# Kernel tuning notes

Measured on AMD Instinct MI355X. Metric: run time of the kernel, lower is better.

The kernel has to match this reference:

```python
import jax, jax.numpy as jnp
import numpy as np

D = 8192          # dimension (high_dim_mode since > 1000)
M = 1_600_000     # ~0.05 * D*(D-1) pairs after the i>j mask
RIEMANN_SHIFT = 0.5


def _lower_tri_pairs(rng, d, m):
    # Sample m unique strictly-lower-triangular (i, j) positions (i > j).
    total = d * (d - 1) // 2
    k = rng.choice(total, size=m, replace=False)
    kf = k.astype(np.float64)
    i = np.floor((1.0 + np.sqrt(1.0 + 8.0 * kf)) / 2.0).astype(np.int64)
    # fix possible off-by-one from float sqrt
    tri = i * (i - 1) // 2
    i = np.where(tri > k, i - 1, i)
    tri = i * (i - 1) // 2
    j = k - tri
    return i, j


def setup_inputs() -> dict:
    key = jax.random.key(0)
    k1, k2 = jax.random.split(key)
    rng = np.random.default_rng(0)

    i, j = _lower_tri_pairs(rng, D, M)
    interaction_indices = jnp.asarray(np.stack([i, j]))  # [2, M] int64

    local_scale = 1.0 / D ** 0.75
    h_local = jax.random.normal(k1, (D,), dtype=jnp.float32) * local_scale + RIEMANN_SHIFT

    dim_factor = 1.0 / (D ** 0.9 * np.log(D))
    V_interaction = jax.random.normal(k2, (M,), dtype=jnp.float32) * dim_factor

    return {
        "h_local": h_local,
        "V_interaction": V_interaction,
        "interaction_indices": interaction_indices,
        "dimension": D,
    }


def reference(h_local, V_interaction, interaction_indices, dimension) -> jnp.ndarray:
    d = h_local.shape[0]
    # scatter interaction values into strict lower triangle (set semantics,
    # indices are unique so set == torch assignment)
    H_int = jnp.zeros((d, d), dtype=h_local.dtype)
    H_int = H_int.at[interaction_indices[0], interaction_indices[1]].set(V_interaction)
    H_int = H_int + H_int.T  # symmetrize
    interaction_scale = 1.0 - 0.2 / np.sqrt(np.log(dimension))
    return jnp.diag(h_local) + H_int * interaction_scale
```

## Files before the change

kernel.cpp:

```cpp
#include <hip/hip_runtime.h>
#include <math.h>


#define P1_PAIRS 4096
#define NBKT     2048
#define BCAP     8
#define NB2      4096
#define OVB      512
#define OVCAP    64
#define SENTK    0xFFFFFFFFu
#define GCAP     65536


__global__ __launch_bounds__(1024) void p1_kernel(
    const int*   __restrict__ idx,
    const float* __restrict__ vals,
    float scale, int m, int nblk,
    uint2* __restrict__ region1,
    uint2* __restrict__ ovfreg,
    int*   __restrict__ ovfcur,
    uint2* __restrict__ glist,
    int*   __restrict__ ghdr)
{
    __shared__ uint2 stage[NBKT][BCAP];
    __shared__ int   cnt[NBKT];
    __shared__ uint2 ovfst[OVB];
    __shared__ int   ovfn;

    uint2* sflat = &stage[0][0];
    for (int f = threadIdx.x; f < NBKT * BCAP; f += 1024)
        sflat[f] = make_uint2(SENTK, 0u);
    for (int b = threadIdx.x; b < NBKT; b += 1024) cnt[b] = 0;
    if (threadIdx.x == 0) ovfn = 0;
    __syncthreads();

    const int blk  = blockIdx.x;
    const int base = blk * P1_PAIRS;
#pragma unroll
    for (int it = 0; it < P1_PAIRS / 1024; ++it) {
        int k = base + it * 1024 + threadIdx.x;
        if (k < m) {
            int i = idx[k];
            int j = idx[m + k];
            unsigned vb = __float_as_uint(vals[k] * scale);

            unsigned k1 = ((unsigned)i << 13) | (unsigned)j;
            int b1 = i >> 2;
            int p = atomicAdd(&cnt[b1], 1);
            if (p < BCAP) stage[b1][p] = make_uint2(k1, vb);
            else { int q = atomicAdd(&ovfn, 1);
                   if (q < OVB) ovfst[q] = make_uint2(k1, vb);
                   else { int g = atomicAdd(ghdr, 1); if (g < GCAP) glist[g] = make_uint2(k1, vb); } }

            unsigned k2 = ((unsigned)j << 13) | (unsigned)i;
            int b2 = j >> 2;
            p = atomicAdd(&cnt[b2], 1);
            if (p < BCAP) stage[b2][p] = make_uint2(k2, vb);
            else { int q = atomicAdd(&ovfn, 1);
                   if (q < OVB) ovfst[q] = make_uint2(k2, vb);
                   else { int g = atomicAdd(ghdr, 1); if (g < GCAP) glist[g] = make_uint2(k2, vb); } }
        }
    }
    __syncthreads();

    for (int f = threadIdx.x; f < NBKT * BCAP; f += 1024) {
        int b = f >> 3, e = f & 7;
        region1[((long long)b * nblk + blk) * BCAP + e] = sflat[f];
    }
    int n = ovfn; if (n > OVB) n = OVB;
    for (int e = threadIdx.x; e < n; e += 1024) {
        uint2 en = ovfst[e];
        int band2 = en.x >> 14;
        int pos = atomicAdd(&ovfcur[band2], 1);
        if (pos < OVCAP) ovfreg[band2 * OVCAP + pos] = en;
        else { int g = atomicAdd(ghdr, 1); if (g < GCAP) glist[g] = en; }
    }
}

__global__ __launch_bounds__(512) void p2_kernel(
    float* __restrict__ out,
    const float* __restrict__ h_local,
    const uint2* __restrict__ region1,
    int nblk,
    const uint2* __restrict__ ovfreg,
    const int*   __restrict__ ovfcur,
    const uint2* __restrict__ glist,
    const int*   __restrict__ ghdr)
{
    __shared__ float srow[2 * 8192];
    float4* s4 = reinterpret_cast<float4*>(srow);
    const int band2 = blockIdx.x;

    for (int c = threadIdx.x; c < 4096; c += 512)
        s4[c] = make_float4(0.f, 0.f, 0.f, 0.f);
    __syncthreads();

    const uint4* src = reinterpret_cast<const uint4*>(
        region1 + (long long)(band2 >> 1) * nblk * BCAP);
    const int n2 = (nblk * BCAP) >> 1;
    const unsigned bu = (unsigned)band2;
    for (int e = threadIdx.x; e < n2; e += 512) {
        uint4 en = src[e];
        if ((en.x >> 14) == bu) srow[en.x & 16383] = __uint_as_float(en.y);
        if ((en.z >> 14) == bu) srow[en.z & 16383] = __uint_as_float(en.w);
    }
    int n = ovfcur[band2]; if (n > OVCAP) n = OVCAP;
    for (int e = threadIdx.x; e < n; e += 512) {
        uint2 en = ovfreg[band2 * OVCAP + e];
        srow[en.x & 16383] = __uint_as_float(en.y);
    }
    int gn = ghdr[0];
    if (gn > 0) {
        if (gn > GCAP) gn = GCAP;
        for (int e = threadIdx.x; e < gn; e += 512) {
            uint2 en = glist[e];
            if ((en.x >> 14) == bu) srow[en.x & 16383] = __uint_as_float(en.y);
        }
    }
    if (threadIdx.x < 2) {
        int r = (band2 << 1) + threadIdx.x;
        srow[((unsigned)threadIdx.x << 13) | (unsigned)r] = h_local[r];
    }
    __syncthreads();

    float4* orow = reinterpret_cast<float4*>(out + ((long long)band2 << 14));
    for (int c = threadIdx.x; c < 4096; c += 512)
        orow[c] = s4[c];
}


__global__ __launch_bounds__(256) void init_counts_kernel(
    float* __restrict__ out, int d, int logd)
{
    int r = blockIdx.x * blockDim.x + threadIdx.x;
    if (r < d) reinterpret_cast<int*>(out)[(long long)r << logd] = 0;
}

__global__ __launch_bounds__(256) void bin_kernel(
    float* __restrict__ out,
    const int*   __restrict__ idx,
    const float* __restrict__ vals,
    float scale, int m, int logd, int cap)
{
    int k = blockIdx.x * blockDim.x + threadIdx.x;
    if (k >= m) return;
    int i = idx[k];
    int j = idx[m + k];
    unsigned vb = __float_as_uint(vals[k] * scale);
    int* cnt_i = reinterpret_cast<int*>(out) + ((long long)i << logd);
    int* cnt_j = reinterpret_cast<int*>(out) + ((long long)j << logd);
    int p1 = atomicAdd(cnt_i, 1);
    if (p1 < cap)
        *reinterpret_cast<uint2*>(out + ((long long)i << logd) + 2 + 2 * p1) =
            make_uint2((unsigned)j, vb);
    int p2 = atomicAdd(cnt_j, 1);
    if (p2 < cap)
        *reinterpret_cast<uint2*>(out + ((long long)j << logd) + 2 + 2 * p2) =
            make_uint2((unsigned)i, vb);
}

__global__ __launch_bounds__(256) void rows_kernel(
    float* __restrict__ out,
    const float* __restrict__ h_local,
    int logd, int cap)
{
    __shared__ float srow[8192];
    const int d  = 1 << logd;
    const int n4 = d >> 2;
    float4* s4 = reinterpret_cast<float4*>(srow);
    const int r = blockIdx.x;
    float* grow = out + ((long long)r << logd);
    const float4 z = make_float4(0.f, 0.f, 0.f, 0.f);
    for (int c = threadIdx.x; c < n4; c += blockDim.x) s4[c] = z;
    __syncthreads();
    int cnt = reinterpret_cast<const int*>(grow)[0];
    if (cnt > cap) cnt = cap;
    const uint2* eb = reinterpret_cast<const uint2*>(grow + 2);
    for (int e = threadIdx.x; e < cnt; e += blockDim.x) {
        uint2 p = eb[e];
        srow[p.x] = __uint_as_float(p.y);
    }
    if (threadIdx.x == 0) srow[r] = h_local[r];
    __syncthreads();
    for (int c = threadIdx.x; c < n4; c += blockDim.x)
        reinterpret_cast<float4*>(grow)[c] = s4[c];
}

__global__ __launch_bounds__(256) void fill_diag_kernel(
    float* __restrict__ out, const float* __restrict__ h_local,
    int d, long long n)
{
    long long t = (long long)blockIdx.x * blockDim.x + threadIdx.x;
    if (t >= n) return;
    long long row = t / d;
    long long col = t - row * d;
    out[t] = (row == col) ? h_local[row] : 0.f;
}

__global__ __launch_bounds__(256) void scatter_kernel(
    float* __restrict__ out,
    const int* __restrict__ idx,
    const float* __restrict__ vals,
    float scale, int m, int d)
{
    int k = blockIdx.x * blockDim.x + threadIdx.x;
    if (k >= m) return;
    int i = idx[k];
    int j = idx[m + k];
    float v = vals[k] * scale;
    out[(long long)i * d + j] = v;
    out[(long long)j * d + i] = v;
}


extern "C" void kernel_launch(void* const* d_in, const int* in_sizes, int n_in,
                              void* d_out, int out_size, void* d_ws, size_t ws_size,
                              hipStream_t stream) {
    const float* h_local = (const float*)d_in[0];
    const float* V_int   = (const float*)d_in[1];
    const int*   idx     = (const int*)d_in[2];

    const int d = in_sizes[0];
    const int m = in_sizes[1];

    int logd = 0;
    while ((1 << logd) < d) ++logd;
    const bool pow2 = ((1 << logd) == d);

    const float iscale = (float)(1.0 - 0.2 / sqrt(log((double)d)));
    float* out = (float*)d_out;
    const int block = 256;

    const int nblk = (m + P1_PAIRS - 1) / P1_PAIRS;

    const size_t off_ovfcur = 4096;
    const size_t hdr_bytes  = off_ovfcur + (size_t)NB2 * 4;
    const size_t off_glist  = 24576;
    const size_t off_ovfreg = off_glist + (size_t)GCAP * sizeof(uint2);
    const size_t off_r1     = off_ovfreg + (size_t)NB2 * OVCAP * sizeof(uint2);
    const size_t ws_need    = off_r1 + (size_t)NBKT * nblk * BCAP * sizeof(uint2);

    const bool path7 = (d == 8192) && (m > 0) && (m <= 2000000) &&
                       (d_ws != nullptr) && (ws_size >= ws_need);

    if (path7) {
        char* ws = (char*)d_ws;
        int*   ghdr    = (int*)ws;
        int*   ovfcur  = (int*)(ws + off_ovfcur);
        uint2* glist   = (uint2*)(ws + off_glist);
        uint2* ovfreg  = (uint2*)(ws + off_ovfreg);
        uint2* region1 = (uint2*)(ws + off_r1);

        hipMemsetAsync(ws, 0, hdr_bytes, stream);
        p1_kernel<<<nblk, 1024, 0, stream>>>(idx, V_int, iscale, m, nblk,
                                             region1, ovfreg, ovfcur, glist, ghdr);
        p2_kernel<<<NB2, 512, 0, stream>>>(out, h_local, region1, nblk,
                                           ovfreg, ovfcur, glist, ghdr);
    } else if (pow2 && d >= 1024 && d <= 8192 &&
               ((long long)m * 2 / d) < (long long)((d - 2) / 2) / 2) {
        const int cap = (d - 2) / 2;
        init_counts_kernel<<<(d + block - 1) / block, block, 0, stream>>>(out, d, logd);
        bin_kernel<<<(m + block - 1) / block, block, 0, stream>>>(out, idx, V_int,
                                                                  iscale, m, logd, cap);
        rows_kernel<<<d, block, 0, stream>>>(out, h_local, logd, cap);
    } else {
        const long long n = (long long)d * d;
        const long long grid_fill = (n + block - 1) / block;
        fill_diag_kernel<<<(dim3)(unsigned)grid_fill, block, 0, stream>>>(out, h_local, d, n);
        const int grid_sc = (m + block - 1) / block;
        scatter_kernel<<<grid_sc, block, 0, stream>>>(out, idx, V_int, iscale, m, d);
    }
}
```

Before: 328.2 us.

## Use fixed chunk count in binning and double-buffer multi-band row assembly

The binning pass now uses a fixed 512 chunks of about 3125 pairs each, two chunks per 1024-thread block, in place of fixed 4096-pair blocks. The row-assembly kernel now handles 16 bands per 1024-thread block and ping-pongs two shared buffers. It writes one band to global memory and zeroes that buffer while gathering the next band into the other. This is meant to cut launch and per-block zero-init overhead and to overlap gather reads with output writes. The risks are 256 p2 blocks, which may leave CUs underused, and the 8-slot buckets, which now see more pairs per chunk and so may overflow more often.

Result: slower. 349.1 us (+6.4%).

```diff
diff --git a/kernel.cpp b/kernel.cpp
--- a/kernel.cpp
+++ b/kernel.cpp
@@ -2,10 +2,11 @@
 #include <math.h>
 
 
-#define P1_PAIRS 4096
+#define NCHUNK   512
 #define NBKT     2048
 #define BCAP     8
 #define NB2      4096
+#define BANDS_PB 16
 #define OVB      512
 #define OVCAP    64
 #define SENTK    0xFFFFFFFFu
@@ -15,7 +16,7 @@
 __global__ __launch_bounds__(1024) void p1_kernel(
     const int*   __restrict__ idx,
     const float* __restrict__ vals,
-    float scale, int m, int nblk,
+    float scale, int m, int cs,
     uint2* __restrict__ region1,
     uint2* __restrict__ ovfreg,
     int*   __restrict__ ovfcur,
@@ -26,20 +27,20 @@
     __shared__ int   cnt[NBKT];
     __shared__ uint2 ovfst[OVB];
     __shared__ int   ovfn;
-
     uint2* sflat = &stage[0][0];
-    for (int f = threadIdx.x; f < NBKT * BCAP; f += 1024)
-        sflat[f] = make_uint2(SENTK, 0u);
-    for (int b = threadIdx.x; b < NBKT; b += 1024) cnt[b] = 0;
-    if (threadIdx.x == 0) ovfn = 0;
-    __syncthreads();
-
-    const int blk  = blockIdx.x;
-    const int base = blk * P1_PAIRS;
-#pragma unroll
-    for (int it = 0; it < P1_PAIRS / 1024; ++it) {
-        int k = base + it * 1024 + threadIdx.x;
-        if (k < m) {
+    const int tid = threadIdx.x;
+
+    for (int c = 0; c < 2; ++c) {
+        const int chunk = blockIdx.x * 2 + c;
+
+        for (int f = tid; f < NBKT * BCAP; f += 1024) sflat[f] = make_uint2(SENTK, 0u);
+        for (int b = tid; b < NBKT; b += 1024) cnt[b] = 0;
+        if (tid == 0) ovfn = 0;
+        __syncthreads();
+
+        const int base = chunk * cs;
+        int end = base + cs; if (end > m) end = m;
+        for (int k = base + tid; k < end; k += 1024) {
             int i = idx[k];
             int j = idx[m + k];
             unsigned vb = __float_as_uint(vals[k] * scale);
@@ -60,72 +61,101 @@
                    if (q < OVB) ovfst[q] = make_uint2(k2, vb);
                    else { int g = atomicAdd(ghdr, 1); if (g < GCAP) glist[g] = make_uint2(k2, vb); } }
         }
-    }
-    __syncthreads();
-
-    for (int f = threadIdx.x; f < NBKT * BCAP; f += 1024) {
-        int b = f >> 3, e = f & 7;
-        region1[((long long)b * nblk + blk) * BCAP + e] = sflat[f];
-    }
-    int n = ovfn; if (n > OVB) n = OVB;
-    for (int e = threadIdx.x; e < n; e += 1024) {
-        uint2 en = ovfst[e];
-        int band2 = en.x >> 14;
-        int pos = atomicAdd(&ovfcur[band2], 1);
-        if (pos < OVCAP) ovfreg[band2 * OVCAP + pos] = en;
-        else { int g = atomicAdd(ghdr, 1); if (g < GCAP) glist[g] = en; }
-    }
-}
-
-__global__ __launch_bounds__(512) void p2_kernel(
+        __syncthreads();
+
+        for (int f = tid; f < NBKT * BCAP; f += 1024) {
+            int bkt = f >> 3, e = f & 7;
+            region1[((long long)bkt * NCHUNK + chunk) * BCAP + e] = sflat[f];
+        }
+        int n = ovfn; if (n > OVB) n = OVB;
+        for (int e = tid; e < n; e += 1024) {
+            uint2 en = ovfst[e];
+            int band = en.x >> 14;
+            int pos = atomicAdd(&ovfcur[band], 1);
+            if (pos < OVCAP) ovfreg[band * OVCAP + pos] = en;
+            else { int g = atomicAdd(ghdr, 1); if (g < GCAP) glist[g] = en; }
+        }
+        __syncthreads();
+    }
+}
+
+__device__ __forceinline__ void gather_band(
+    float* __restrict__ buf,
+    int band,
+    const uint2* __restrict__ region1,
+    const uint2* __restrict__ ovfreg,
+    const int*   __restrict__ ovfcur,
+    const uint2* __restrict__ glist,
+    int gn,
+    const float* __restrict__ h_local,
+    int tid)
+{
+    const uint4* src = reinterpret_cast<const uint4*>(
+        region1 + (long long)(band >> 1) * NCHUNK * BCAP);
+    const unsigned bu = (unsigned)band;
+    for (int e = tid; e < (NCHUNK * BCAP) / 2; e += 1024) {
+        uint4 en = src[e];
+        if ((en.x >> 14) == bu) buf[en.x & 16383] = __uint_as_float(en.y);
+        if ((en.z >> 14) == bu) buf[en.z & 16383] = __uint_as_float(en.w);
+    }
+    int n = ovfcur[band]; if (n > OVCAP) n = OVCAP;
+    for (int e = tid; e < n; e += 1024) {
+        uint2 en = ovfreg[band * OVCAP + e];
+        buf[en.x & 16383] = __uint_as_float(en.y);
+    }
+    if (gn > 0) {
+        for (int e = tid; e < gn; e += 1024) {
+            uint2 en = glist[e];
+            if ((en.x >> 14) == bu) buf[en.x & 16383] = __uint_as_float(en.y);
+        }
+    }
+    if (tid < 2) {
+        int r = (band << 1) + tid;
+        buf[((unsigned)tid << 13) | (unsigned)r] = h_local[r];
+    }
+}
+
+__global__ __launch_bounds__(1024) void p2_kernel(
     float* __restrict__ out,
     const float* __restrict__ h_local,
     const uint2* __restrict__ region1,
-    int nblk,
     const uint2* __restrict__ ovfreg,
     const int*   __restrict__ ovfcur,
     const uint2* __restrict__ glist,
     const int*   __restrict__ ghdr)
 {
-    __shared__ float srow[2 * 8192];
-    float4* s4 = reinterpret_cast<float4*>(srow);
-    const int band2 = blockIdx.x;
-
-    for (int c = threadIdx.x; c < 4096; c += 512)
-        s4[c] = make_float4(0.f, 0.f, 0.f, 0.f);
+    __shared__ float bufA[16384];
+    __shared__ float bufB[16384];
+    const int tid = threadIdx.x;
+    const int b0  = blockIdx.x * BANDS_PB;
+
+    int gn = ghdr[0]; if (gn > GCAP) gn = GCAP;
+
+    float4* a4 = reinterpret_cast<float4*>(bufA);
+    float4* b4 = reinterpret_cast<float4*>(bufB);
+    const float4 z = make_float4(0.f, 0.f, 0.f, 0.f);
+    for (int c = tid; c < 4096; c += 1024) { a4[c] = z; b4[c] = z; }
     __syncthreads();
 
-    const uint4* src = reinterpret_cast<const uint4*>(
-        region1 + (long long)(band2 >> 1) * nblk * BCAP);
-    const int n2 = (nblk * BCAP) >> 1;
-    const unsigned bu = (unsigned)band2;
-    for (int e = threadIdx.x; e < n2; e += 512) {
-        uint4 en = src[e];
-        if ((en.x >> 14) == bu) srow[en.x & 16383] = __uint_as_float(en.y);
-        if ((en.z >> 14) == bu) srow[en.z & 16383] = __uint_as_float(en.w);
-    }
-    int n = ovfcur[band2]; if (n > OVCAP) n = OVCAP;
-    for (int e = threadIdx.x; e < n; e += 512) {
-        uint2 en = ovfreg[band2 * OVCAP + e];
-        srow[en.x & 16383] = __uint_as_float(en.y);
-    }
-    int gn = ghdr[0];
-    if (gn > 0) {
-        if (gn > GCAP) gn = GCAP;
-        for (int e = threadIdx.x; e < gn; e += 512) {
-            uint2 en = glist[e];
-            if ((en.x >> 14) == bu) srow[en.x & 16383] = __uint_as_float(en.y);
-        }
-    }
-    if (threadIdx.x < 2) {
-        int r = (band2 << 1) + threadIdx.x;
-        srow[((unsigned)threadIdx.x << 13) | (unsigned)r] = h_local[r];
-    }
+    gather_band(bufA, b0, region1, ovfreg, ovfcur, glist, gn, h_local, tid);
     __syncthreads();
 
-    float4* orow = reinterpret_cast<float4*>(out + ((long long)band2 << 14));
-    for (int c = threadIdx.x; c < 4096; c += 512)
-        orow[c] = s4[c];
+    for (int t = 0; t < BANDS_PB; ++t) {
+        float4* cur = (t & 1) ? b4 : a4;
+        float4* nxt = (t & 1) ? a4 : b4;
+        const int band = b0 + t;
+
+        float4* orow = reinterpret_cast<float4*>(out + ((long long)band << 14));
+        for (int c = tid; c < 4096; c += 1024) {
+            float4 v = cur[c];
+            orow[c] = v;
+            cur[c] = z;
+        }
+        if (t + 1 < BANDS_PB)
+            gather_band(reinterpret_cast<float*>(nxt), band + 1,
+                        region1, ovfreg, ovfcur, glist, gn, h_local, tid);
+        __syncthreads();
+    }
 }
 
 
@@ -231,19 +261,17 @@
     float* out = (float*)d_out;
     const int block = 256;
 
-    const int nblk = (m + P1_PAIRS - 1) / P1_PAIRS;
-
     const size_t off_ovfcur = 4096;
     const size_t hdr_bytes  = off_ovfcur + (size_t)NB2 * 4;
     const size_t off_glist  = 24576;
     const size_t off_ovfreg = off_glist + (size_t)GCAP * sizeof(uint2);
     const size_t off_r1     = off_ovfreg + (size_t)NB2 * OVCAP * sizeof(uint2);
-    const size_t ws_need    = off_r1 + (size_t)NBKT * nblk * BCAP * sizeof(uint2);
-
-    const bool path7 = (d == 8192) && (m > 0) && (m <= 2000000) &&
+    const size_t ws_need    = off_r1 + (size_t)NBKT * NCHUNK * BCAP * sizeof(uint2);
+
+    const bool path8 = (d == 8192) && (m > 0) && (m <= 2200000) &&
                        (d_ws != nullptr) && (ws_size >= ws_need);
 
-    if (path7) {
+    if (path8) {
         char* ws = (char*)d_ws;
         int*   ghdr    = (int*)ws;
         int*   ovfcur  = (int*)(ws + off_ovfcur);
@@ -251,11 +279,14 @@
         uint2* ovfreg  = (uint2*)(ws + off_ovfreg);
         uint2* region1 = (uint2*)(ws + off_r1);
 
+        const int cs = (m + NCHUNK - 1) / NCHUNK;
+
         hipMemsetAsync(ws, 0, hdr_bytes, stream);
-        p1_kernel<<<nblk, 1024, 0, stream>>>(idx, V_int, iscale, m, nblk,
-                                             region1, ovfreg, ovfcur, glist, ghdr);
-        p2_kernel<<<NB2, 512, 0, stream>>>(out, h_local, region1, nblk,
-                                           ovfreg, ovfcur, glist, ghdr);
+        p1_kernel<<<NCHUNK / 2, 1024, 0, stream>>>(idx, V_int, iscale, m, cs,
+                                                   region1, ovfreg, ovfcur,
+                                                   glist, ghdr);
+        p2_kernel<<<NB2 / BANDS_PB, 1024, 0, stream>>>(out, h_local, region1,
+                                                       ovfreg, ovfcur, glist, ghdr);
     } else if (pow2 && d >= 1024 && d <= 8192 &&
                ((long long)m * 2 / d) < (long long)((d - 2) / 2) / 2) {
         const int cap = (d - 2) / 2;
```
